# Kernel tuning notes

Measured on AMD Instinct MI355X. Metric: run time of the kernel, lower is better.

## Reference

```python
import jax, jax.numpy as jnp
import numpy as np

N_NODES = 100000
N_EDGES = 1600000
IN_FEATS = 256
OUT_FEATS = 64


def setup_inputs() -> dict:
    key = jax.random.key(0)
    k1, k2, k3, k4, k5 = jax.random.split(key, 5)
    feat = jax.random.normal(k1, (N_NODES, IN_FEATS), dtype=jnp.float32)
    W = jax.random.normal(k2, (IN_FEATS, OUT_FEATS), dtype=jnp.float32)
    ew = jax.random.uniform(k3, (N_EDGES,), dtype=jnp.float32)
    src = jax.random.randint(k4, (N_EDGES,), 0, N_NODES, dtype=jnp.int64)
    dst = jax.random.randint(k5, (N_EDGES,), 0, N_NODES, dtype=jnp.int64)
    return {"feat": feat, "W": W, "ew": ew, "src": src, "dst": dst}


def reference(feat, W, ew, src, dst):
    # h = feat @ W  (node-level projection)
    h = feat @ W                              # [N, out]
    # src_mul_edge: m_e = h[src_e] * w_e ; fn.sum: h_v = sum_{e: dst_e=v} m_e
    msg = h[src] * ew[:, None]                # [E, out]
    agg = jax.ops.segment_sum(msg, dst, num_segments=N_NODES)  # [N, out]
    return jax.nn.relu(agg)
```

## Files before the change

### kernel.cpp

```cpp
#include <hip/hip_runtime.h>

#define IN_F 256
#define OUT_F 64
#define LOGSB 8
#define SBNODES 256
#define MAXSB 1024

typedef __bf16 bf16x8 __attribute__((ext_vector_type(8)));
typedef float f32x4 __attribute__((ext_vector_type(4)));

__global__ __launch_bounds__(64) void wfrag_kernel(const float* __restrict__ W,
                                                   __bf16* __restrict__ wfrag,
                                                   int* __restrict__ bcnt,
                                                   int* __restrict__ sbcur, int nsb) {
    const int st = blockIdx.x;
    const int l = threadIdx.x;
    if (st == 0)
        for (int i = l; i <= nsb; i += 64) bcnt[i] = 0;
    if (st == 1)
        for (int i = l; i < nsb; i += 64) sbcur[i] = 0;
    const int s = st >> 2, t = st & 3;
    const int n = t * 16 + (l & 15);
    const int k0 = s * 32 + (l >> 4) * 8;
    bf16x8 f;
#pragma unroll
    for (int j = 0; j < 8; ++j)
        f[j] = (__bf16)W[(k0 + j) * OUT_F + n];
    *(bf16x8*)(wfrag + (size_t)(st * 64 + l) * 8) = f;
}

__global__ __launch_bounds__(256) void gemmhist_kernel(const float* __restrict__ feat,
                                                       const __bf16* __restrict__ wfrag,
                                                       __bf16* __restrict__ h, int N,
                                                       const int* __restrict__ dst,
                                                       int* __restrict__ bcnt, int E, int nsb,
                                                       int gemmBlocks) {
    __shared__ int histo[MAXSB];
    if ((int)blockIdx.x < gemmBlocks) {
        const int tid = threadIdx.x;
        const int wv = tid >> 6;
        const int l = tid & 63;
        const int m0 = blockIdx.x * 64 + wv * 16;
        const int q = l >> 4;
        const int row = min(m0 + (l & 15), N - 1);

        const float* __restrict__ arow = feat + (size_t)row * IN_F + q * 8;
        const bf16x8* __restrict__ wf = (const bf16x8*)wfrag;

        f32x4 acc0 = {0.f, 0.f, 0.f, 0.f};
        f32x4 acc1 = {0.f, 0.f, 0.f, 0.f};
        f32x4 acc2 = {0.f, 0.f, 0.f, 0.f};
        f32x4 acc3 = {0.f, 0.f, 0.f, 0.f};

#pragma unroll
        for (int s = 0; s < 8; ++s) {
            float4 fa0 = *(const float4*)(arow + s * 32);
            float4 fa1 = *(const float4*)(arow + s * 32 + 4);
            bf16x8 a;
            a[0] = (__bf16)fa0.x; a[1] = (__bf16)fa0.y;
            a[2] = (__bf16)fa0.z; a[3] = (__bf16)fa0.w;
            a[4] = (__bf16)fa1.x; a[5] = (__bf16)fa1.y;
            a[6] = (__bf16)fa1.z; a[7] = (__bf16)fa1.w;
            bf16x8 b0 = wf[(s * 4 + 0) * 64 + l];
            bf16x8 b1 = wf[(s * 4 + 1) * 64 + l];
            bf16x8 b2 = wf[(s * 4 + 2) * 64 + l];
            bf16x8 b3 = wf[(s * 4 + 3) * 64 + l];
            acc0 = __builtin_amdgcn_mfma_f32_16x16x32_bf16(a, b0, acc0, 0, 0, 0);
            acc1 = __builtin_amdgcn_mfma_f32_16x16x32_bf16(a, b1, acc1, 0, 0, 0);
            acc2 = __builtin_amdgcn_mfma_f32_16x16x32_bf16(a, b2, acc2, 0, 0, 0);
            acc3 = __builtin_amdgcn_mfma_f32_16x16x32_bf16(a, b3, acc3, 0, 0, 0);
        }

        const int colb = l & 15;
#pragma unroll
        for (int r = 0; r < 4; ++r) {
            int ro = m0 + q * 4 + r;
            if (ro < N) {
                __bf16* hp = h + (size_t)ro * OUT_F + colb;
                hp[0]  = (__bf16)acc0[r];
                hp[16] = (__bf16)acc1[r];
                hp[32] = (__bf16)acc2[r];
                hp[48] = (__bf16)acc3[r];
            }
        }
    } else {
        const int hb = blockIdx.x - gemmBlocks;
        const int nhb = gridDim.x - gemmBlocks;
        for (int i = threadIdx.x; i < nsb; i += 256) histo[i] = 0;
        __syncthreads();
        const int stride = nhb * 1024;
        for (int base = (hb * 256 + threadIdx.x) * 4; base < E; base += stride) {
            if (base + 4 <= E) {
                int4 d4 = *(const int4*)(dst + base);
                atomicAdd(&histo[d4.x >> LOGSB], 1);
                atomicAdd(&histo[d4.y >> LOGSB], 1);
                atomicAdd(&histo[d4.z >> LOGSB], 1);
                atomicAdd(&histo[d4.w >> LOGSB], 1);
            } else {
                for (int e = base; e < E; ++e) atomicAdd(&histo[dst[e] >> LOGSB], 1);
            }
        }
        __syncthreads();
        for (int i = threadIdx.x; i < nsb; i += 256)
            if (histo[i]) atomicAdd(&bcnt[i], histo[i]);
    }
}

__global__ __launch_bounds__(1024) void sbscatter_kernel(const int* __restrict__ src,
                                                         const int* __restrict__ dst,
                                                         const float* __restrict__ ew,
                                                         const int* __restrict__ bcnt,
                                                         int* __restrict__ sbcur,
                                                         int2* __restrict__ payload,
                                                         int E, int nsb) {
    __shared__ int s[1024];
    __shared__ int sbb[MAXSB];
    __shared__ int cnt[MAXSB];
    __shared__ int basearr[MAXSB];
    const int t = threadIdx.x;

    int v = (t < nsb) ? bcnt[t] : 0;
    s[t] = v;
    __syncthreads();
    for (int o = 1; o < 1024; o <<= 1) {
        int x = (t >= o) ? s[t - o] : 0;
        __syncthreads();
        s[t] += x;
        __syncthreads();
    }
    if (t < nsb) sbb[t] = s[t] - v;
    for (int i = t; i < nsb; i += 1024) cnt[i] = 0;
    __syncthreads();

    const int base = (blockIdx.x * 1024 + t) * 8;
    int dd[8], ss[8];
    float ww[8];
    int nv = 0;
    if (base + 8 <= E) {
        int4 d4a = *(const int4*)(dst + base);
        int4 d4b = *(const int4*)(dst + base + 4);
        int4 s4a = *(const int4*)(src + base);
        int4 s4b = *(const int4*)(src + base + 4);
        float4 w4a = *(const float4*)(ew + base);
        float4 w4b = *(const float4*)(ew + base + 4);
        dd[0] = d4a.x; dd[1] = d4a.y; dd[2] = d4a.z; dd[3] = d4a.w;
        dd[4] = d4b.x; dd[5] = d4b.y; dd[6] = d4b.z; dd[7] = d4b.w;
        ss[0] = s4a.x; ss[1] = s4a.y; ss[2] = s4a.z; ss[3] = s4a.w;
        ss[4] = s4b.x; ss[5] = s4b.y; ss[6] = s4b.z; ss[7] = s4b.w;
        ww[0] = w4a.x; ww[1] = w4a.y; ww[2] = w4a.z; ww[3] = w4a.w;
        ww[4] = w4b.x; ww[5] = w4b.y; ww[6] = w4b.z; ww[7] = w4b.w;
        nv = 8;
    } else if (base < E) {
        nv = E - base;
#pragma unroll 8
        for (int j = 0; j < 8; ++j)
            if (j < nv) { dd[j] = dst[base + j]; ss[j] = src[base + j]; ww[j] = ew[base + j]; }
    }

    int idx[8];
#pragma unroll 8
    for (int j = 0; j < 8; ++j)
        if (j < nv) idx[j] = atomicAdd(&cnt[dd[j] >> LOGSB], 1);
    __syncthreads();

    for (int i = t; i < nsb; i += 1024)
        if (cnt[i]) basearr[i] = sbb[i] + atomicAdd(&sbcur[i], cnt[i]);
    __syncthreads();

#pragma unroll 8
    for (int j = 0; j < 8; ++j)
        if (j < nv) {
            int pos = basearr[dd[j] >> LOGSB] + idx[j];
            payload[pos] = make_int2(ss[j] | ((dd[j] & (SBNODES - 1)) << 24),
                                     __float_as_int(ww[j]));
        }
}

__global__ __launch_bounds__(256) void fsort_kernel(const int2* __restrict__ payload,
                                                    unsigned* __restrict__ payload2,
                                                    const int* __restrict__ bcnt,
                                                    int* __restrict__ noff,
                                                    int N, int E, int nsb) {
    __shared__ int red[256];
    __shared__ int cnt[SBNODES];
    __shared__ int off[SBNODES + 1];
    __shared__ int tick[SBNODES];
    const int t = threadIdx.x;
    const int bid = blockIdx.x;

    int partial = 0;
    for (int i = t; i < bid; i += 256) partial += bcnt[i];
    red[t] = partial;
    __syncthreads();
    for (int o = 128; o > 0; o >>= 1) {
        if (t < o) red[t] += red[t + o];
        __syncthreads();
    }
    const int b = red[0];
    const int m = bcnt[bid];
    const int mlim = min(m, 4096);

    int2 ed[16];
#pragma unroll
    for (int k = 0; k < 16; ++k) {
        int i = t + k * 256;
        if (i < mlim) ed[k] = payload[b + i];
    }

    cnt[t] = 0;
    __syncthreads();
#pragma unroll
    for (int k = 0; k < 16; ++k) {
        int i = t + k * 256;
        if (i < mlim) atomicAdd(&cnt[((unsigned)ed[k].x) >> 24], 1);
    }
    for (int i = 4096 + t; i < m; i += 256)
        atomicAdd(&cnt[((unsigned)payload[b + i].x) >> 24], 1);
    __syncthreads();

    if (t == 0) off[0] = 0;
    off[t + 1] = cnt[t];
    __syncthreads();
    for (int o = 1; o < SBNODES; o <<= 1) {
        int v2 = (t >= o) ? off[t + 1 - o] : 0;
        __syncthreads();
        off[t + 1] += v2;
        __syncthreads();
    }

    const int g = (bid << LOGSB) + t;
    if (g < N) noff[g] = b + off[t];
    if (bid == 0 && t == 0) noff[N] = E;
    tick[t] = 0;
    __syncthreads();

#pragma unroll
    for (int k = 0; k < 16; ++k) {
        int i = t + k * 256;
        if (i < mlim) {
            int2 p = ed[k];
            int ld = ((unsigned)p.x) >> 24;
            int pos = b + off[ld] + atomicAdd(&tick[ld], 1);
            unsigned wb = (unsigned)p.y;
            unsigned b16 = (wb + 0x7FFFu + ((wb >> 16) & 1u)) >> 16;
            payload2[pos] = (((unsigned)(p.x & 0xFFFFFF)) << 15) | (b16 & 0x7FFFu);
        }
    }
    for (int i = 4096 + t; i < m; i += 256) {
        int2 p = payload[b + i];
        int ld = ((unsigned)p.x) >> 24;
        int pos = b + off[ld] + atomicAdd(&tick[ld], 1);
        unsigned wb = (unsigned)p.y;
        unsigned b16 = (wb + 0x7FFFu + ((wb >> 16) & 1u)) >> 16;
        payload2[pos] = (((unsigned)(p.x & 0xFFFFFF)) << 15) | (b16 & 0x7FFFu);
    }
}

#define EDGE8P(PBASE, A0A, A0B, A1A, A1B, A2A, A2B, A3A, A3B)                   \
    {                                                                           \
        unsigned p0 = (PBASE)[0];                                               \
        unsigned p1 = (PBASE)[1];                                               \
        unsigned p2 = (PBASE)[2];                                               \
        unsigned p3 = (PBASE)[3];                                               \
        unsigned p4 = (PBASE)[4];                                               \
        unsigned p5 = (PBASE)[5];                                               \
        unsigned p6 = (PBASE)[6];                                               \
        unsigned p7 = (PBASE)[7];                                               \
        unsigned v0 = h32[(size_t)(p0 >> 15) * 32 + j];                         \
        unsigned v1 = h32[(size_t)(p1 >> 15) * 32 + j];                         \
        unsigned v2 = h32[(size_t)(p2 >> 15) * 32 + j];                         \
        unsigned v3 = h32[(size_t)(p3 >> 15) * 32 + j];                         \
        unsigned v4 = h32[(size_t)(p4 >> 15) * 32 + j];                         \
        unsigned v5 = h32[(size_t)(p5 >> 15) * 32 + j];                         \
        unsigned v6 = h32[(size_t)(p6 >> 15) * 32 + j];                         \
        unsigned v7 = h32[(size_t)(p7 >> 15) * 32 + j];                         \
        float w0 = __uint_as_float((p0 & 0x7FFFu) << 16);                       \
        float w1 = __uint_as_float((p1 & 0x7FFFu) << 16);                       \
        float w2 = __uint_as_float((p2 & 0x7FFFu) << 16);                       \
        float w3 = __uint_as_float((p3 & 0x7FFFu) << 16);                       \
        float w4 = __uint_as_float((p4 & 0x7FFFu) << 16);                       \
        float w5 = __uint_as_float((p5 & 0x7FFFu) << 16);                       \
        float w6 = __uint_as_float((p6 & 0x7FFFu) << 16);                       \
        float w7 = __uint_as_float((p7 & 0x7FFFu) << 16);                       \
        A0A = fmaf(__uint_as_float(v0 << 16), w0, A0A);                         \
        A0B = fmaf(__uint_as_float(v0 & 0xFFFF0000u), w0, A0B);                 \
        A1A = fmaf(__uint_as_float(v1 << 16), w1, A1A);                         \
        A1B = fmaf(__uint_as_float(v1 & 0xFFFF0000u), w1, A1B);                 \
        A2A = fmaf(__uint_as_float(v2 << 16), w2, A2A);                         \
        A2B = fmaf(__uint_as_float(v2 & 0xFFFF0000u), w2, A2B);                 \
        A3A = fmaf(__uint_as_float(v3 << 16), w3, A3A);                         \
        A3B = fmaf(__uint_as_float(v3 & 0xFFFF0000u), w3, A3B);                 \
        A0A = fmaf(__uint_as_float(v4 << 16), w4, A0A);                         \
        A0B = fmaf(__uint_as_float(v4 & 0xFFFF0000u), w4, A0B);                 \
        A1A = fmaf(__uint_as_float(v5 << 16), w5, A1A);                         \
        A1B = fmaf(__uint_as_float(v5 & 0xFFFF0000u), w5, A1B);                 \
        A2A = fmaf(__uint_as_float(v6 << 16), w6, A2A);                         \
        A2B = fmaf(__uint_as_float(v6 & 0xFFFF0000u), w6, A2B);                 \
        A3A = fmaf(__uint_as_float(v7 << 16), w7, A3A);                         \
        A3B = fmaf(__uint_as_float(v7 & 0xFFFF0000u), w7, A3B);                 \
    }

__global__ __launch_bounds__(256) void bgather_kernel(const __bf16* __restrict__ h,
                                                      const unsigned* __restrict__ payload2,
                                                      const int* __restrict__ noff,
                                                      float* __restrict__ out, int N) {
    const int t = threadIdx.x;
    const int hw = t >> 5;
    const int j = t & 31;
    const unsigned* __restrict__ h32 = (const unsigned*)h;
    const int g0 = blockIdx.x * 32;

#pragma unroll 1
    for (int k = 0; k < 4; ++k) {
        const int g = g0 + hw + k * 8;
        if (g >= N) continue;
        int i = noff[g];
        const int eE = noff[g + 1];
        float a0A = 0.f, a0B = 0.f, a1A = 0.f, a1B = 0.f;
        float a2A = 0.f, a2B = 0.f, a3A = 0.f, a3B = 0.f;
        float b0A = 0.f, b0B = 0.f, b1A = 0.f, b1B = 0.f;
        float b2A = 0.f, b2B = 0.f, b3A = 0.f, b3B = 0.f;
#pragma unroll 1
        for (; i + 16 <= eE; i += 16) {
            EDGE8P(payload2 + i, a0A, a0B, a1A, a1B, a2A, a2B, a3A, a3B)
            EDGE8P(payload2 + i + 8, b0A, b0B, b1A, b1B, b2A, b2B, b3A, b3B)
        }
        if (i + 8 <= eE) {
            EDGE8P(payload2 + i, a0A, a0B, a1A, a1B, a2A, a2B, a3A, a3B)
            i += 8;
        }
        for (; i + 2 <= eE; i += 2) {
            unsigned p0 = payload2[i + 0];
            unsigned p1 = payload2[i + 1];
            unsigned v0 = h32[(size_t)(p0 >> 15) * 32 + j];
            unsigned v1 = h32[(size_t)(p1 >> 15) * 32 + j];
            float w0 = __uint_as_float((p0 & 0x7FFFu) << 16);
            float w1 = __uint_as_float((p1 & 0x7FFFu) << 16);
            a0A = fmaf(__uint_as_float(v0 << 16), w0, a0A);
            a0B = fmaf(__uint_as_float(v0 & 0xFFFF0000u), w0, a0B);
            a1A = fmaf(__uint_as_float(v1 << 16), w1, a1A);
            a1B = fmaf(__uint_as_float(v1 & 0xFFFF0000u), w1, a1B);
        }
        if (i < eE) {
            unsigned p0 = payload2[i];
            unsigned v0 = h32[(size_t)(p0 >> 15) * 32 + j];
            float w0 = __uint_as_float((p0 & 0x7FFFu) << 16);
            a0A = fmaf(__uint_as_float(v0 << 16), w0, a0A);
            a0B = fmaf(__uint_as_float(v0 & 0xFFFF0000u), w0, a0B);
        }
        float2 v;
        v.x = fmaxf(((a0A + a1A) + (a2A + a3A)) + ((b0A + b1A) + (b2A + b3A)), 0.f);
        v.y = fmaxf(((a0B + a1B) + (a2B + a3B)) + ((b0B + b1B) + (b2B + b3B)), 0.f);
        *(float2*)(out + (size_t)g * OUT_F + 2 * j) = v;
    }
}

extern "C" void kernel_launch(void* const* d_in, const int* in_sizes, int n_in,
                              void* d_out, int out_size, void* d_ws, size_t ws_size,
                              hipStream_t stream) {
    const float* feat = (const float*)d_in[0];
    const float* W    = (const float*)d_in[1];
    const float* ew   = (const float*)d_in[2];
    const int*   src  = (const int*)d_in[3];
    const int*   dst  = (const int*)d_in[4];
    float* out = (float*)d_out;

    const int N = in_sizes[0] / IN_F;
    const int E = in_sizes[2];
    const int nsb = (N + SBNODES - 1) >> LOGSB;

    char* ws = (char*)d_ws;
    int2*     payload  = (int2*)ws;     ws += (size_t)E * 8;
    unsigned* payload2 = (unsigned*)ws; ws += (size_t)E * 4;
    __bf16*   h        = (__bf16*)ws;   ws += (size_t)N * OUT_F * 2;
    __bf16*   wfrag    = (__bf16*)ws;   ws += 32 * 64 * 8 * 2;
    int*      bcnt     = (int*)ws;      ws += (MAXSB + 1) * 4;
    int*      sbcur    = (int*)ws;      ws += MAXSB * 4;
    int*      noff     = (int*)ws;

    const int gemmBlocks = (N + 63) / 64;

    hipLaunchKernelGGL(wfrag_kernel, dim3(32), dim3(64), 0, stream, W, wfrag, bcnt, sbcur, nsb);
    hipLaunchKernelGGL(gemmhist_kernel, dim3(gemmBlocks + 512), dim3(256), 0, stream,
                       feat, wfrag, h, N, dst, bcnt, E, nsb, gemmBlocks);
    hipLaunchKernelGGL(sbscatter_kernel, dim3((E + 8191) / 8192), dim3(1024), 0, stream,
                       src, dst, ew, bcnt, sbcur, payload, E, nsb);
    hipLaunchKernelGGL(fsort_kernel, dim3(nsb), dim3(256), 0, stream,
                       payload, payload2, bcnt, noff, N, E, nsb);
    hipLaunchKernelGGL(bgather_kernel, dim3((N + 31) / 32), dim3(256), 0, stream,
                       h, payload2, noff, out, N);
}
```

Baseline: 117.7 us.

## Move GEMM alongside edge scatter and split histogram into its own kernel

The dst histogram now runs alone in its own kernel. The node projection GEMM is fused into the scatter launch, so the GEMM blocks overlap with the edge bucketing instead of with the histogram. Scatter blocks shrink from 1024 to 256 threads, each handling 16 edges. The prefix scan is rewritten to match the smaller block. The aim is to balance work across the launches, because the histogram is light and the scatter is heavy. The cost is one more kernel launch, and scan overhead is repeated in each of the roughly 390 scatter blocks.

Measured after the change: 132.9 us. +13.0%, slower.

```diff
diff --git a/kernel.cpp b/kernel.cpp
--- a/kernel.cpp
+++ b/kernel.cpp
@@ -29,18 +29,119 @@
     *(bf16x8*)(wfrag + (size_t)(st * 64 + l) * 8) = f;
 }
 
-__global__ __launch_bounds__(256) void gemmhist_kernel(const float* __restrict__ feat,
+__global__ __launch_bounds__(256) void sbhist_kernel(const int* __restrict__ dst,
+                                                     int* __restrict__ bcnt, int E, int nsb) {
+    __shared__ int histo[MAXSB];
+    for (int i = threadIdx.x; i < nsb; i += 256) histo[i] = 0;
+    __syncthreads();
+    const int stride = gridDim.x * 1024;
+    for (int base = (blockIdx.x * 256 + threadIdx.x) * 4; base < E; base += stride) {
+        if (base + 4 <= E) {
+            int4 d4 = *(const int4*)(dst + base);
+            atomicAdd(&histo[d4.x >> LOGSB], 1);
+            atomicAdd(&histo[d4.y >> LOGSB], 1);
+            atomicAdd(&histo[d4.z >> LOGSB], 1);
+            atomicAdd(&histo[d4.w >> LOGSB], 1);
+        } else {
+            for (int e = base; e < E; ++e) atomicAdd(&histo[dst[e] >> LOGSB], 1);
+        }
+    }
+    __syncthreads();
+    for (int i = threadIdx.x; i < nsb; i += 256)
+        if (histo[i]) atomicAdd(&bcnt[i], histo[i]);
+}
+
+__global__ __launch_bounds__(256) void scatgemm_kernel(const int* __restrict__ src,
+                                                       const int* __restrict__ dst,
+                                                       const float* __restrict__ ew,
+                                                       const int* __restrict__ bcnt,
+                                                       int* __restrict__ sbcur,
+                                                       int2* __restrict__ payload,
+                                                       int E, int nsb,
+                                                       const float* __restrict__ feat,
                                                        const __bf16* __restrict__ wfrag,
                                                        __bf16* __restrict__ h, int N,
-                                                       const int* __restrict__ dst,
-                                                       int* __restrict__ bcnt, int E, int nsb,
-                                                       int gemmBlocks) {
-    __shared__ int histo[MAXSB];
-    if ((int)blockIdx.x < gemmBlocks) {
-        const int tid = threadIdx.x;
-        const int wv = tid >> 6;
-        const int l = tid & 63;
-        const int m0 = blockIdx.x * 64 + wv * 16;
+                                                       int scatBlocks) {
+    __shared__ int s[256];
+    __shared__ int sbb[MAXSB];
+    __shared__ int cnt[MAXSB];
+    __shared__ int basearr[MAXSB];
+    const int t = threadIdx.x;
+
+    if ((int)blockIdx.x < scatBlocks) {
+        int v[4];
+        int sum = 0;
+#pragma unroll
+        for (int q = 0; q < 4; ++q) {
+            int i = 4 * t + q;
+            v[q] = (i < nsb) ? bcnt[i] : 0;
+            sum += v[q];
+        }
+        s[t] = sum;
+        __syncthreads();
+        for (int o = 1; o < 256; o <<= 1) {
+            int x = (t >= o) ? s[t - o] : 0;
+            __syncthreads();
+            s[t] += x;
+            __syncthreads();
+        }
+        int ex = s[t] - sum;
+#pragma unroll
+        for (int q = 0; q < 4; ++q) {
+            int i = 4 * t + q;
+            if (i < nsb) sbb[i] = ex;
+            ex += v[q];
+        }
+        for (int i = t; i < nsb; i += 256) cnt[i] = 0;
+        __syncthreads();
+
+        const int base = blockIdx.x * 4096 + t * 16;
+        int dd[16], ss[16];
+        float ww[16];
+        int nv = 0;
+        if (base + 16 <= E) {
+#pragma unroll
+            for (int q = 0; q < 4; ++q) {
+                int4 d4 = *(const int4*)(dst + base + q * 4);
+                int4 s4 = *(const int4*)(src + base + q * 4);
+                float4 w4 = *(const float4*)(ew + base + q * 4);
+                dd[q * 4 + 0] = d4.x; dd[q * 4 + 1] = d4.y;
+                dd[q * 4 + 2] = d4.z; dd[q * 4 + 3] = d4.w;
+                ss[q * 4 + 0] = s4.x; ss[q * 4 + 1] = s4.y;
+                ss[q * 4 + 2] = s4.z; ss[q * 4 + 3] = s4.w;
+                ww[q * 4 + 0] = w4.x; ww[q * 4 + 1] = w4.y;
+                ww[q * 4 + 2] = w4.z; ww[q * 4 + 3] = w4.w;
+            }
+            nv = 16;
+        } else if (base < E) {
+            nv = E - base;
+#pragma unroll 16
+            for (int q = 0; q < 16; ++q)
+                if (q < nv) { dd[q] = dst[base + q]; ss[q] = src[base + q]; ww[q] = ew[base + q]; }
+        }
+
+        int idx[16];
+#pragma unroll 16
+        for (int q = 0; q < 16; ++q)
+            if (q < nv) idx[q] = atomicAdd(&cnt[dd[q] >> LOGSB], 1);
+        __syncthreads();
+
+        for (int i = t; i < nsb; i += 256)
+            if (cnt[i]) basearr[i] = sbb[i] + atomicAdd(&sbcur[i], cnt[i]);
+        __syncthreads();
+
+#pragma unroll 16
+        for (int q = 0; q < 16; ++q)
+            if (q < nv) {
+                int pos = basearr[dd[q] >> LOGSB] + idx[q];
+                payload[pos] = make_int2(ss[q] | ((dd[q] & (SBNODES - 1)) << 24),
+                                         __float_as_int(ww[q]));
+            }
+    } else {
+        const int gb = blockIdx.x - scatBlocks;
+        const int wv = t >> 6;
+        const int l = t & 63;
+        const int m0 = gb * 64 + wv * 16;
         const int q = l >> 4;
         const int row = min(m0 + (l & 15), N - 1);
 
@@ -53,18 +154,18 @@
         f32x4 acc3 = {0.f, 0.f, 0.f, 0.f};
 
 #pragma unroll
-        for (int s = 0; s < 8; ++s) {
-            float4 fa0 = *(const float4*)(arow + s * 32);
-            float4 fa1 = *(const float4*)(arow + s * 32 + 4);
+        for (int sK = 0; sK < 8; ++sK) {
+            float4 fa0 = *(const float4*)(arow + sK * 32);
+            float4 fa1 = *(const float4*)(arow + sK * 32 + 4);
             bf16x8 a;
             a[0] = (__bf16)fa0.x; a[1] = (__bf16)fa0.y;
             a[2] = (__bf16)fa0.z; a[3] = (__bf16)fa0.w;
             a[4] = (__bf16)fa1.x; a[5] = (__bf16)fa1.y;
             a[6] = (__bf16)fa1.z; a[7] = (__bf16)fa1.w;
-            bf16x8 b0 = wf[(s * 4 + 0) * 64 + l];
-            bf16x8 b1 = wf[(s * 4 + 1) * 64 + l];
-            bf16x8 b2 = wf[(s * 4 + 2) * 64 + l];
-            bf16x8 b3 = wf[(s * 4 + 3) * 64 + l];
+            bf16x8 b0 = wf[(sK * 4 + 0) * 64 + l];
+            bf16x8 b1 = wf[(sK * 4 + 1) * 64 + l];
+            bf16x8 b2 = wf[(sK * 4 + 2) * 64 + l];
+            bf16x8 b3 = wf[(sK * 4 + 3) * 64 + l];
             acc0 = __builtin_amdgcn_mfma_f32_16x16x32_bf16(a, b0, acc0, 0, 0, 0);
             acc1 = __builtin_amdgcn_mfma_f32_16x16x32_bf16(a, b1, acc1, 0, 0, 0);
             acc2 = __builtin_amdgcn_mfma_f32_16x16x32_bf16(a, b2, acc2, 0, 0, 0);
@@ -83,97 +184,7 @@
                 hp[48] = (__bf16)acc3[r];
             }
         }
-    } else {
-        const int hb = blockIdx.x - gemmBlocks;
-        const int nhb = gridDim.x - gemmBlocks;
-        for (int i = threadIdx.x; i < nsb; i += 256) histo[i] = 0;
-        __syncthreads();
-        const int stride = nhb * 1024;
-        for (int base = (hb * 256 + threadIdx.x) * 4; base < E; base += stride) {
-            if (base + 4 <= E) {
-                int4 d4 = *(const int4*)(dst + base);
-                atomicAdd(&histo[d4.x >> LOGSB], 1);
-                atomicAdd(&histo[d4.y >> LOGSB], 1);
-                atomicAdd(&histo[d4.z >> LOGSB], 1);
-                atomicAdd(&histo[d4.w >> LOGSB], 1);
-            } else {
-                for (int e = base; e < E; ++e) atomicAdd(&histo[dst[e] >> LOGSB], 1);
-            }
-        }
-        __syncthreads();
-        for (int i = threadIdx.x; i < nsb; i += 256)
-            if (histo[i]) atomicAdd(&bcnt[i], histo[i]);
-    }
-}
-
-__global__ __launch_bounds__(1024) void sbscatter_kernel(const int* __restrict__ src,
-                                                         const int* __restrict__ dst,
-                                                         const float* __restrict__ ew,
-                                                         const int* __restrict__ bcnt,
-                                                         int* __restrict__ sbcur,
-                                                         int2* __restrict__ payload,
-                                                         int E, int nsb) {
-    __shared__ int s[1024];
-    __shared__ int sbb[MAXSB];
-    __shared__ int cnt[MAXSB];
-    __shared__ int basearr[MAXSB];
-    const int t = threadIdx.x;
-
-    int v = (t < nsb) ? bcnt[t] : 0;
-    s[t] = v;
-    __syncthreads();
-    for (int o = 1; o < 1024; o <<= 1) {
-        int x = (t >= o) ? s[t - o] : 0;
-        __syncthreads();
-        s[t] += x;
-        __syncthreads();
-    }
-    if (t < nsb) sbb[t] = s[t] - v;
-    for (int i = t; i < nsb; i += 1024) cnt[i] = 0;
-    __syncthreads();
-
-    const int base = (blockIdx.x * 1024 + t) * 8;
-    int dd[8], ss[8];
-    float ww[8];
-    int nv = 0;
-    if (base + 8 <= E) {
-        int4 d4a = *(const int4*)(dst + base);
-        int4 d4b = *(const int4*)(dst + base + 4);
-        int4 s4a = *(const int4*)(src + base);
-        int4 s4b = *(const int4*)(src + base + 4);
-        float4 w4a = *(const float4*)(ew + base);
-        float4 w4b = *(const float4*)(ew + base + 4);
-        dd[0] = d4a.x; dd[1] = d4a.y; dd[2] = d4a.z; dd[3] = d4a.w;
-        dd[4] = d4b.x; dd[5] = d4b.y; dd[6] = d4b.z; dd[7] = d4b.w;
-        ss[0] = s4a.x; ss[1] = s4a.y; ss[2] = s4a.z; ss[3] = s4a.w;
-        ss[4] = s4b.x; ss[5] = s4b.y; ss[6] = s4b.z; ss[7] = s4b.w;
-        ww[0] = w4a.x; ww[1] = w4a.y; ww[2] = w4a.z; ww[3] = w4a.w;
-        ww[4] = w4b.x; ww[5] = w4b.y; ww[6] = w4b.z; ww[7] = w4b.w;
-        nv = 8;
-    } else if (base < E) {
-        nv = E - base;
-#pragma unroll 8
-        for (int j = 0; j < 8; ++j)
-            if (j < nv) { dd[j] = dst[base + j]; ss[j] = src[base + j]; ww[j] = ew[base + j]; }
-    }
-
-    int idx[8];
-#pragma unroll 8
-    for (int j = 0; j < 8; ++j)
-        if (j < nv) idx[j] = atomicAdd(&cnt[dd[j] >> LOGSB], 1);
-    __syncthreads();
-
-    for (int i = t; i < nsb; i += 1024)
-        if (cnt[i]) basearr[i] = sbb[i] + atomicAdd(&sbcur[i], cnt[i]);
-    __syncthreads();
-
-#pragma unroll 8
-    for (int j = 0; j < 8; ++j)
-        if (j < nv) {
-            int pos = basearr[dd[j] >> LOGSB] + idx[j];
-            payload[pos] = make_int2(ss[j] | ((dd[j] & (SBNODES - 1)) << 24),
-                                     __float_as_int(ww[j]));
-        }
+    }
 }
 
 __global__ __launch_bounds__(256) void fsort_kernel(const int2* __restrict__ payload,
@@ -379,12 +390,13 @@
     int*      noff     = (int*)ws;
 
     const int gemmBlocks = (N + 63) / 64;
+    const int scatBlocks = (E + 4095) / 4096;
 
     hipLaunchKernelGGL(wfrag_kernel, dim3(32), dim3(64), 0, stream, W, wfrag, bcnt, sbcur, nsb);
-    hipLaunchKernelGGL(gemmhist_kernel, dim3(gemmBlocks + 512), dim3(256), 0, stream,
-                       feat, wfrag, h, N, dst, bcnt, E, nsb, gemmBlocks);
-    hipLaunchKernelGGL(sbscatter_kernel, dim3((E + 8191) / 8192), dim3(1024), 0, stream,
-                       src, dst, ew, bcnt, sbcur, payload, E, nsb);
+    hipLaunchKernelGGL(sbhist_kernel, dim3(512), dim3(256), 0, stream, dst, bcnt, E, nsb);
+    hipLaunchKernelGGL(scatgemm_kernel, dim3(scatBlocks + gemmBlocks), dim3(256), 0, stream,
+                       src, dst, ew, bcnt, sbcur, payload, E, nsb,
+                       feat, wfrag, h, N, scatBlocks);
     hipLaunchKernelGGL(fsort_kernel, dim3(nsb), dim3(256), 0, stream,
                        payload, payload2, bcnt, noff, N, E, nsb);
     hipLaunchKernelGGL(bgather_kernel, dim3((N + 31) / 32), dim3(256), 0, stream,
```
